# Kernel optimization log

Hardware: AMD Instinct MI355X
Metric: run time of the kernel (lower is better)

The kernel has to match this reference:

```python
import jax, jax.numpy as jnp
import numpy as np
from jax import lax

H = 145; W = 145; BANDS = 200; D_MODEL = 128; NUM_CLASSES = 17
# Mamba2 defaults: expand=2, headdim=64, d_state=128, d_conv=4, ngroups=1
D_INNER = 256; NHEADS = 4; HEADDIM = 64; D_STATE = 128; D_CONV = 4
D_IN_PROJ = 2 * D_INNER + 2 * D_STATE + NHEADS  # 772
CONV_DIM = D_INNER + 2 * D_STATE                # 512


def _gelu(x):
    return jax.nn.gelu(x, approximate=False)


def _ln(x, g, b, eps=1e-5):
    m = jnp.mean(x, -1, keepdims=True)
    v = jnp.mean((x - m) ** 2, -1, keepdims=True)
    return (x - m) * lax.rsqrt(v + eps) * g + b


def _adaptive_pool_last(x, out):
    # PyTorch AdaptiveAvgPool semantics along the last axis via integral image
    L = x.shape[-1]
    i = np.arange(out)
    starts = (i * L) // out
    ends = -((-(i + 1) * L) // out)  # ceil((i+1)*L/out)
    cs = jnp.concatenate([jnp.zeros(x.shape[:-1] + (1,), x.dtype), jnp.cumsum(x, -1)], -1)
    return (cs[..., ends] - cs[..., starts]) / jnp.asarray(ends - starts, x.dtype)


def _mamba2(u, in_w, conv_w, conv_b, dt_bias, A_log, D, norm_w, out_w):
    # u: (L, D_MODEL). Faithful Mamba2 reference path (batch=1 squeezed).
    L = u.shape[0]
    zxbcdt = u @ in_w                      # (L, 772)
    z = zxbcdt[:, :D_INNER]                # (L, 256)
    xBC = zxbcdt[:, D_INNER:2 * D_INNER + 2 * D_STATE]  # (L, 512)
    dt = jax.nn.softplus(zxbcdt[:, -NHEADS:] + dt_bias)  # (L, 4)
    # causal depthwise conv1d, kernel D_CONV, then SiLU
    xp = jnp.pad(xBC, ((D_CONV - 1, 0), (0, 0)))
    xBC = sum(xp[k:k + L] * conv_w[:, k] for k in range(D_CONV)) + conv_b
    xBC = jax.nn.silu(xBC)
    xh = xBC[:, :D_INNER].reshape(L, NHEADS, HEADDIM)     # (L, h, p)
    Bm = xBC[:, D_INNER:D_INNER + D_STATE]                # (L, n)
    Cm = xBC[:, D_INNER + D_STATE:]                       # (L, n)
    A = -jnp.exp(A_log)                                   # (h,)

    def step(state, inp):
        dt_t, x_t, B_t, C_t = inp          # (h,), (h,p), (n,), (n,)
        dA = jnp.exp(dt_t * A)             # (h,)
        state = state * dA[:, None, None] + (dt_t[:, None] * x_t)[:, :, None] * B_t[None, None, :]
        y_t = jnp.einsum('hpn,n->hp', state, C_t)
        return state, y_t

    s0 = jnp.zeros((NHEADS, HEADDIM, D_STATE), u.dtype)
    _, y = lax.scan(step, s0, (dt, xh, Bm, Cm))           # y: (L, h, p)
    y = y + D[None, :, None] * xh
    y = y.reshape(L, D_INNER) * jax.nn.silu(z)            # gated
    y = y * lax.rsqrt(jnp.mean(y * y, -1, keepdims=True) + 1e-5) * norm_w  # RMSNormGated
    return y @ out_w                                      # (L, D_MODEL)


def _forward(x, ln_pre_g, ln_pre_b, fe_w1, fe_b1, fe_w2, fe_b2,
             cv_w1, cv_b1, cv_w2, cv_b2, mp_w, mp_b, mp_ln_g, mp_ln_b,
             m_in_w, m_conv_w, m_conv_b, m_dt_bias, m_A_log, m_D, m_norm_w, m_out_w,
             cls_ln_g, cls_ln_b, cls_w1, cls_b1, cls_w2, cls_b2, cls_w3, cls_b3):
    h, w, _ = x.shape
    xn = _ln(x, ln_pre_g, ln_pre_b)
    # MLP feature branch
    f = _gelu(xn @ fe_w1 + fe_b1)
    f = _gelu(f @ fe_w2 + fe_b2)                          # (h, w, 128)
    # conv branch
    c = jnp.transpose(xn, (2, 0, 1))[None]                # (1, bands, h, w)
    dn = ('NCHW', 'OIHW', 'NCHW')
    c = lax.conv_general_dilated(c, cv_w1, (1, 1), [(2, 2), (2, 2)], dimension_numbers=dn)
    c = _gelu(c + cv_b1[None, :, None, None])             # (1, 32, 147, 147)
    c = lax.conv_general_dilated(c, cv_w2, (1, 1), [(1, 1), (1, 1)], dimension_numbers=dn)
    c = _gelu(c + cv_b2[None, :, None, None])             # (1, 64, 147, 147)
    c = _adaptive_pool_last(c, W)                         # pool width -> 145
    c = _adaptive_pool_last(c.swapaxes(-1, -2), H).swapaxes(-1, -2)  # pool height
    conv_feat = jnp.transpose(c[0], (1, 2, 0))            # (145, 145, 64)
    comb = jnp.concatenate([f, conv_feat], -1).reshape(h * w, 192)
    p = _gelu(_ln(comb @ mp_w + mp_b, mp_ln_g, mp_ln_b))  # (L, d_model)
    m = _mamba2(p, m_in_w, m_conv_w, m_conv_b, m_dt_bias, m_A_log, m_D, m_norm_w, m_out_w)
    r = m.reshape(h, w, D_MODEL)
    o = _ln(r, cls_ln_g, cls_ln_b)
    o = _gelu(o @ cls_w1 + cls_b1)
    o = _gelu(o @ cls_w2 + cls_b2)
    return o @ cls_w3 + cls_b3                            # (h, w, num_classes)


def setup_inputs() -> dict:
    key = jax.random.key(0)
    ks = jax.random.split(key, 16)
    def n(k, shape, s=0.02):
        return jax.random.normal(k, shape, jnp.float32) * s
    return dict(
        x=jax.random.normal(ks[0], (H, W, BANDS), jnp.float32),
        ln_pre_g=jnp.ones((BANDS,), jnp.float32), ln_pre_b=jnp.zeros((BANDS,), jnp.float32),
        fe_w1=n(ks[1], (BANDS, 256)), fe_b1=jnp.zeros((256,), jnp.float32),
        fe_w2=n(ks[2], (256, 128)), fe_b2=jnp.zeros((128,), jnp.float32),
        cv_w1=n(ks[3], (32, BANDS, 3, 3)), cv_b1=jnp.zeros((32,), jnp.float32),
        cv_w2=n(ks[4], (64, 32, 3, 3)), cv_b2=jnp.zeros((64,), jnp.float32),
        mp_w=n(ks[5], (192, D_MODEL)), mp_b=jnp.zeros((D_MODEL,), jnp.float32),
        mp_ln_g=jnp.ones((D_MODEL,), jnp.float32), mp_ln_b=jnp.zeros((D_MODEL,), jnp.float32),
        m_in_w=n(ks[6], (D_MODEL, D_IN_PROJ)),
        m_conv_w=n(ks[7], (CONV_DIM, D_CONV), 0.2), m_conv_b=jnp.zeros((CONV_DIM,), jnp.float32),
        m_dt_bias=jnp.full((NHEADS,), -4.0, jnp.float32),
        m_A_log=jnp.log(jnp.linspace(1.0, 16.0, NHEADS)).astype(jnp.float32),
        m_D=jnp.ones((NHEADS,), jnp.float32),
        m_norm_w=jnp.ones((D_INNER,), jnp.float32),
        m_out_w=n(ks[8], (D_INNER, D_MODEL)),
        cls_ln_g=jnp.ones((D_MODEL,), jnp.float32), cls_ln_b=jnp.zeros((D_MODEL,), jnp.float32),
        cls_w1=n(ks[9], (D_MODEL, 128)), cls_b1=jnp.zeros((128,), jnp.float32),
        cls_w2=n(ks[10], (128, 64)), cls_b2=jnp.zeros((64,), jnp.float32),
        cls_w3=n(ks[11], (64, NUM_CLASSES)), cls_b3=jnp.zeros((NUM_CLASSES,), jnp.float32),
    )


def reference(x, ln_pre_g, ln_pre_b, fe_w1, fe_b1, fe_w2, fe_b2,
              cv_w1, cv_b1, cv_w2, cv_b2, mp_w, mp_b, mp_ln_g, mp_ln_b,
              m_in_w, m_conv_w, m_conv_b, m_dt_bias, m_A_log, m_D, m_norm_w, m_out_w,
              cls_ln_g, cls_ln_b, cls_w1, cls_b1, cls_w2, cls_b2, cls_w3, cls_b3):
    return _forward(x, ln_pre_g, ln_pre_b, fe_w1, fe_b1, fe_w2, fe_b2,
                    cv_w1, cv_b1, cv_w2, cv_b2, mp_w, mp_b, mp_ln_g, mp_ln_b,
                    m_in_w, m_conv_w, m_conv_b, m_dt_bias, m_A_log, m_D, m_norm_w, m_out_w,
                    cls_ln_g, cls_ln_b, cls_w1, cls_b1, cls_w2, cls_b2, cls_w3, cls_b3)
```

## Files before the change

kernel.cpp:

```cpp
#include <hip/hip_runtime.h>
#include <math.h>

#define HW 21025
#define Hdim 145
#define Wdim 145
#define NBANDS 200
#define CONVH 147
#define CONVHW 21609
#define QC 64
#define NCH 329
#define DTP 21056
#define SP 72
#define SSD_GRID 1344
#define NYB165 165

typedef __attribute__((ext_vector_type(4))) float fv4;
typedef __attribute__((ext_vector_type(8))) short short8;

#define OFF_XN   ((size_t)0)
#define OFF_F1   ((size_t)4205000)
#define OFF_COMB ((size_t)9587400)
#define OFF_P    ((size_t)13624200)
#define OFF_ZX   ((size_t)16315400)
#define OFF_XBC  ((size_t)32546700)
#define OFF_S    ((size_t)43311500)
#define OFF_DT   ((size_t)54092172)
#define OFF_CT   ((size_t)54176396)
#define OFF_W    ((size_t)54177712)

__device__ __forceinline__ float gelu_f(float x){
    return 0.5f * x * (1.0f + erff(x * 0.70710678118654752440f));
}
__device__ __forceinline__ float silu_f(float x){
    return x / (1.0f + expf(-x));
}

__device__ __forceinline__ void bf16_split(float x, unsigned short& hs, unsigned short& ls){
    unsigned u = __float_as_uint(x);
    hs = (unsigned short)(u >> 16);
    float hif = __uint_as_float(u & 0xFFFF0000u);
    float lof = x - hif;
    ls = (unsigned short)(__float_as_uint(lof) >> 16);
}
__device__ __forceinline__ unsigned pack2(unsigned short a, unsigned short b){
    return (unsigned)a | ((unsigned)b << 16);
}
__device__ __forceinline__ unsigned packsplit(float x){
    unsigned short hs, ls;
    bf16_split(x, hs, ls);
    return ((unsigned)hs << 16) | (unsigned)ls;
}
__device__ __forceinline__ float unpackf(unsigned u){
    return __uint_as_float(u & 0xFFFF0000u) + __uint_as_float(u << 16);
}
__device__ __forceinline__ void split8g(const float* p, short8& h8, short8& l8){
    fv4 v0 = *reinterpret_cast<const fv4*>(p);
    fv4 v1 = *reinterpret_cast<const fv4*>(p + 4);
    unsigned short hs, ls;
    #pragma unroll
    for (int j = 0; j < 4; j++){
        bf16_split(v0[j], hs, ls); h8[j] = (short)hs; l8[j] = (short)ls;
        bf16_split(v1[j], hs, ls); h8[4 + j] = (short)hs; l8[4 + j] = (short)ls;
    }
}
__device__ __forceinline__ void unpack8(const unsigned* p, short8& h8, short8& l8){
    uint4 a = *reinterpret_cast<const uint4*>(p);
    uint4 b = *reinterpret_cast<const uint4*>(p + 4);
    unsigned v0 = a.x, v1 = a.y, v2 = a.z, v3 = a.w;
    unsigned v4 = b.x, v5 = b.y, v6 = b.z, v7 = b.w;
    h8[0]=(short)(v0>>16); l8[0]=(short)(v0&0xFFFFu);
    h8[1]=(short)(v1>>16); l8[1]=(short)(v1&0xFFFFu);
    h8[2]=(short)(v2>>16); l8[2]=(short)(v2&0xFFFFu);
    h8[3]=(short)(v3>>16); l8[3]=(short)(v3&0xFFFFu);
    h8[4]=(short)(v4>>16); l8[4]=(short)(v4&0xFFFFu);
    h8[5]=(short)(v5>>16); l8[5]=(short)(v5&0xFFFFu);
    h8[6]=(short)(v6>>16); l8[6]=(short)(v6&0xFFFFu);
    h8[7]=(short)(v7>>16); l8[7]=(short)(v7&0xFFFFu);
}

__device__ __forceinline__ bool gemm_decode(int bid, int NXB, int NYB, int& bx, int& by){
    int m = bid & 7;
    int r = bid >> 3;
    bx = r % NXB;
    by = (r / NXB) * 8 + m;
    return by < NYB;
}
__host__ __forceinline__ int gemm_grid(int NXB, int NYB){ return 8 * ((NYB + 7) / 8) * NXB; }

template<int ACT>
__global__ void ln_kernel(const float* __restrict__ in, const float* __restrict__ g,
                          const float* __restrict__ b, float* __restrict__ out, int D){
    int row = blockIdx.x, tid = threadIdx.x;
    const float* r = in + (size_t)row * D;
    float s = 0.f, s2 = 0.f;
    for (int i = tid; i < D; i += 256){ float v = r[i]; s += v; s2 += v*v; }
    __shared__ float r1[4], r2[4];
    #pragma unroll
    for (int o = 32; o > 0; o >>= 1){ s += __shfl_down(s, o); s2 += __shfl_down(s2, o); }
    if ((tid & 63) == 0){ r1[tid >> 6] = s; r2[tid >> 6] = s2; }
    __syncthreads();
    float S = r1[0] + r1[1] + r1[2] + r1[3];
    float S2 = r2[0] + r2[1] + r2[2] + r2[3];
    float mean = S / (float)D;
    float var = S2 / (float)D - mean * mean;
    float rs = rsqrtf(fmaxf(var, 0.f) + 1e-5f);
    float* o_ = out + (size_t)row * D;
    for (int i = tid; i < D; i += 256){
        float v = (r[i] - mean) * rs * g[i] + b[i];
        if (ACT == 1) v = gelu_f(v);
        o_[i] = v;
    }
}

template<int ACT>
__global__ __launch_bounds__(256) void gemm_mfma(const float* __restrict__ A, int lda,
                                                 const float* __restrict__ B,
                                                 const float* __restrict__ bias,
                                                 float* __restrict__ C, int ldc,
                                                 int M, int N, int K, int NXB, int NYB){
    const int SA = 40;
    __shared__ __align__(16) unsigned short Ah[128 * SA], Al[128 * SA];
    __shared__ __align__(16) unsigned short Bh[64 * SA],  Bl[64 * SA];
    int bx, by;
    if (!gemm_decode(blockIdx.x, NXB, NYB, bx, by)) return;
    int tid = threadIdx.x;
    int lane = tid & 63, wid = tid >> 6;
    int wy = wid >> 1, wx = wid & 1;
    int bm = by * 128, bn = bx * 64;
    int l15 = lane & 15, g = lane >> 4;

    fv4 acc[4][2];
    #pragma unroll
    for (int i = 0; i < 4; i++)
        #pragma unroll
        for (int j = 0; j < 2; j++) acc[i][j] = (fv4){0.f,0.f,0.f,0.f};

    int am = tid >> 1;
    int aq = (tid & 1) * 4;
    bool arow_ok = (bm + am) < M;
    int bn_t = tid & 63;
    int bk8 = (tid >> 6) * 8;
    bool bcol_ok = (bn + bn_t) < N;

    int nK = (K + 31) / 32;
    for (int ks = 0; ks < nK; ks++){
        int k0 = ks * 32;
        const float* Ap = A + (size_t)(bm + am) * lda + k0;
        #pragma unroll
        for (int f = 0; f < 4; f++){
            int kq = aq + f;
            fv4 v = (fv4){0.f,0.f,0.f,0.f};
            if (arow_ok && (k0 + kq * 4 + 4) <= K)
                v = *reinterpret_cast<const fv4*>(Ap + kq * 4);
            unsigned short hs[4], ls[4];
            #pragma unroll
            for (int j = 0; j < 4; j++) bf16_split(v[j], hs[j], ls[j]);
            unsigned off = am * SA + kq * 4;
            *reinterpret_cast<uint2*>(&Ah[off]) = make_uint2(pack2(hs[0],hs[1]), pack2(hs[2],hs[3]));
            *reinterpret_cast<uint2*>(&Al[off]) = make_uint2(pack2(ls[0],ls[1]), pack2(ls[2],ls[3]));
        }
        {
            unsigned short hs[8], ls[8];
            #pragma unroll
            for (int j = 0; j < 8; j++){
                int kk = k0 + bk8 + j;
                float v = (bcol_ok && kk < K) ? B[(size_t)kk * N + bn + bn_t] : 0.f;
                bf16_split(v, hs[j], ls[j]);
            }
            unsigned off = bn_t * SA + bk8;
            *reinterpret_cast<uint4*>(&Bh[off]) = make_uint4(pack2(hs[0],hs[1]), pack2(hs[2],hs[3]),
                                                             pack2(hs[4],hs[5]), pack2(hs[6],hs[7]));
            *reinterpret_cast<uint4*>(&Bl[off]) = make_uint4(pack2(ls[0],ls[1]), pack2(ls[2],ls[3]),
                                                             pack2(ls[4],ls[5]), pack2(ls[6],ls[7]));
        }
        __syncthreads();
        short8 afh[4], afl[4], bfh[2], bfl[2];
        #pragma unroll
        for (int mi = 0; mi < 4; mi++){
            unsigned off = (wy * 64 + mi * 16 + l15) * SA + g * 8;
            afh[mi] = *reinterpret_cast<const short8*>(&Ah[off]);
            afl[mi] = *reinterpret_cast<const short8*>(&Al[off]);
        }
        #pragma unroll
        for (int ni = 0; ni < 2; ni++){
            unsigned off = (wx * 32 + ni * 16 + l15) * SA + g * 8;
            bfh[ni] = *reinterpret_cast<const short8*>(&Bh[off]);
            bfl[ni] = *reinterpret_cast<const short8*>(&Bl[off]);
        }
        #pragma unroll
        for (int mi = 0; mi < 4; mi++)
            #pragma unroll
            for (int ni = 0; ni < 2; ni++){
                acc[mi][ni] = __builtin_amdgcn_mfma_f32_16x16x32_bf16(afh[mi], bfh[ni], acc[mi][ni], 0, 0, 0);
                acc[mi][ni] = __builtin_amdgcn_mfma_f32_16x16x32_bf16(afh[mi], bfl[ni], acc[mi][ni], 0, 0, 0);
                acc[mi][ni] = __builtin_amdgcn_mfma_f32_16x16x32_bf16(afl[mi], bfh[ni], acc[mi][ni], 0, 0, 0);
            }
        __syncthreads();
    }
    #pragma unroll
    for (int mi = 0; mi < 4; mi++){
        #pragma unroll
        for (int ni = 0; ni < 2; ni++){
            int cc = bn + wx * 32 + ni * 16 + l15;
            if (cc >= N) continue;
            float bv = bias ? bias[cc] : 0.f;
            #pragma unroll
            for (int j = 0; j < 4; j++){
                int rr = bm + wy * 64 + mi * 16 + g * 4 + j;
                if (rr >= M) continue;
                float v = acc[mi][ni][j] + bv;
                if (ACT == 1) v = gelu_f(v);
                C[(size_t)rr * ldc + cc] = v;
            }
        }
    }
}

template<int IC, int OC, int NCHUNK>
__global__ void prep_w(const float* __restrict__ w, unsigned short* __restrict__ Wh,
                       unsigned short* __restrict__ Wl){
    const int KP = NCHUNK * 288;
    int idx = blockIdx.x * 256 + threadIdx.x;
    if (idx >= OC * KP) return;
    int o = idx / KP, k = idx % KP;
    int ch = k / 288, rest = k % 288, t = rest / 32, c = rest & 31;
    int ci = ch * 32 + c;
    float v = (ci < IC) ? w[((size_t)o * IC + ci) * 9 + t] : 0.f;
    unsigned short hs, ls;
    bf16_split(v, hs, ls);
    Wh[idx] = hs; Wl[idx] = ls;
}

template<int IC, int OC, int PAD, int NCHUNK, int NFRAG>
__global__ __launch_bounds__(256) void conv_mfma(const float* __restrict__ in,
                                                 int inH, int inW,
                                                 const unsigned short* __restrict__ Wh,
                                                 const unsigned short* __restrict__ Wl,
                                                 const float* __restrict__ bias,
                                                 float* __restrict__ out){
    const int KP = NCHUNK * 288;
    const int CST = 40;
    __shared__ __align__(16) unsigned short Xh[3 * 68 * CST], Xl[3 * 68 * CST];
    int y = blockIdx.y;
    int x0 = blockIdx.x * 64;
    int tid = threadIdx.x;
    int lane = tid & 63, wid = tid >> 6;
    int wy = wid >> 1, wx = wid & 1;
    int l15 = lane & 15, g = lane >> 4;

    fv4 acc[2][NFRAG];
    #pragma unroll
    for (int mi = 0; mi < 2; mi++)
        #pragma unroll
        for (int ni = 0; ni < NFRAG; ni++) acc[mi][ni] = (fv4){0.f,0.f,0.f,0.f};

    for (int ch = 0; ch < NCHUNK; ch++){
        int ci0 = ch * 32;
        if (ch > 0) __syncthreads();
        for (int e = tid; e < 3 * 68 * 8; e += 256){
            int qd = e & 7;
            int c  = (e >> 3) % 68;
            int r  = e / 544;
            int iy = y - PAD + r, ix = x0 - PAD + c;
            fv4 v = (fv4){0.f,0.f,0.f,0.f};
            if ((unsigned)iy < (unsigned)inH && (unsigned)ix < (unsigned)inW &&
                (ci0 + qd * 4 + 4) <= IC)
                v = *reinterpret_cast<const fv4*>(in + ((size_t)iy * inW + ix) * IC + ci0 + qd * 4);
            unsigned short hs[4], ls[4];
            #pragma unroll
            for (int j = 0; j < 4; j++) bf16_split(v[j], hs[j], ls[j]);
            unsigned off = (r * 68 + c) * CST + qd * 4;
            *reinterpret_cast<uint2*>(&Xh[off]) = make_uint2(pack2(hs[0],hs[1]), pack2(hs[2],hs[3]));
            *reinterpret_cast<uint2*>(&Xl[off]) = make_uint2(pack2(ls[0],ls[1]), pack2(ls[2],ls[3]));
        }
        __syncthreads();
        #pragma unroll
        for (int t = 0; t < 9; t++){
            int ky = t / 3, kx = t % 3;
            short8 ah[2], al[2], bh[NFRAG], bl[NFRAG];
            #pragma unroll
            for (int mi = 0; mi < 2; mi++){
                unsigned off = (ky * 68 + wy * 32 + mi * 16 + l15 + kx) * CST + g * 8;
                ah[mi] = *reinterpret_cast<const short8*>(&Xh[off]);
                al[mi] = *reinterpret_cast<const short8*>(&Xl[off]);
            }
            #pragma unroll
            for (int ni = 0; ni < NFRAG; ni++){
                int oc = wx * (16 * NFRAG) + ni * 16 + l15;
                size_t woff = (size_t)oc * KP + ch * 288 + t * 32 + g * 8;
                bh[ni] = *reinterpret_cast<const short8*>(&Wh[woff]);
                bl[ni] = *reinterpret_cast<const short8*>(&Wl[woff]);
            }
            #pragma unroll
            for (int mi = 0; mi < 2; mi++)
                #pragma unroll
                for (int ni = 0; ni < NFRAG; ni++){
                    acc[mi][ni] = __builtin_amdgcn_mfma_f32_16x16x32_bf16(ah[mi], bh[ni], acc[mi][ni], 0, 0, 0);
                    acc[mi][ni] = __builtin_amdgcn_mfma_f32_16x16x32_bf16(ah[mi], bl[ni], acc[mi][ni], 0, 0, 0);
                    acc[mi][ni] = __builtin_amdgcn_mfma_f32_16x16x32_bf16(al[mi], bh[ni], acc[mi][ni], 0, 0, 0);
                }
        }
    }
    #pragma unroll
    for (int mi = 0; mi < 2; mi++)
        #pragma unroll
        for (int ni = 0; ni < NFRAG; ni++){
            int oc = wx * (16 * NFRAG) + ni * 16 + l15;
            float bv = bias[oc];
            #pragma unroll
            for (int j = 0; j < 4; j++){
                int x = x0 + wy * 32 + mi * 16 + g * 4 + j;
                if (x >= CONVH) continue;
                out[((size_t)y * CONVH + x) * OC + oc] = gelu_f(acc[mi][ni][j] + bv);
            }
        }
}

__global__ void pool_kernel(const float* __restrict__ c2, float* __restrict__ comb){
    int idx = blockIdx.x * 256 + threadIdx.x;
    if (idx >= HW * 64) return;
    int o = idx & 63;
    int pix = idx >> 6;
    int xo = pix % Wdim, yo = pix / Wdim;
    int ys = yo * CONVH / Hdim, ye = ((yo + 1) * CONVH + Hdim - 1) / Hdim;
    int xs = xo * CONVH / Wdim, xe = ((xo + 1) * CONVH + Wdim - 1) / Wdim;
    float s = 0.f;
    for (int yy = ys; yy < ye; yy++)
        for (int xx = xs; xx < xe; xx++)
            s += c2[((size_t)yy * CONVH + xx) * 64 + o];
    comb[(size_t)pix * 192 + 128 + o] = s / (float)((ye - ys) * (xe - xs));
}

__global__ void dt_kernel(const float* __restrict__ zx, const float* __restrict__ dt_bias,
                          float* __restrict__ dtbT){
    int t = blockIdx.x * 256 + threadIdx.x;
    int h = blockIdx.y;
    if (t >= HW) return;
    float v = zx[(size_t)t * 772 + 768 + h] + dt_bias[h];
    dtbT[h * DTP + t] = (v > 20.f) ? v : log1pf(expf(v));
}

__global__ __launch_bounds__(256) void conv1d_tiled(const float* __restrict__ zx,
                                                    const float* __restrict__ w,
                                                    const float* __restrict__ b,
                                                    unsigned* __restrict__ xbcp){
    __shared__ float xs[67 * 128];
    __shared__ float wc[4 * 128];
    __shared__ float bc[128];
    int t0 = blockIdx.y * 64;
    int c0 = blockIdx.x * 128;
    int tid = threadIdx.x;
    for (int e = tid; e < 67 * 128; e += 256){
        int rr = e >> 7, cc = e & 127;
        int t = t0 - 3 + rr;
        xs[e] = (t >= 0 && t < HW) ? zx[(size_t)t * 772 + 256 + c0 + cc] : 0.f;
    }
    if (tid < 128){
        bc[tid] = b[c0 + tid];
        #pragma unroll
        for (int k = 0; k < 4; k++) wc[k * 128 + tid] = w[(c0 + tid) * 4 + k];
    }
    __syncthreads();
    for (int e = tid; e < 64 * 128; e += 256){
        int tt = e >> 7, cc = e & 127;
        if (t0 + tt >= HW) continue;
        float acc = bc[cc];
        #pragma unroll
        for (int k = 0; k < 4; k++) acc += xs[(tt + k) * 128 + cc] * wc[k * 128 + cc];
        xbcp[(size_t)(t0 + tt) * 512 + c0 + cc] = packsplit(silu_f(acc));
    }
}

__device__ __forceinline__ void chunk_cumsum_t(const float* __restrict__ dtbT, int t0, int Q,
                                               int h, const float* __restrict__ A_log,
                                               float* cum, float* dth){
    int tid = threadIdx.x;
    if (tid < 64){
        float d = (tid < Q) ? dtbT[h * DTP + t0 + tid] : 0.f;
        dth[tid] = d;
        float A = -expf(A_log[h]);
        float a = d * A;
        #pragma unroll
        for (int off = 1; off < 64; off <<= 1){
            float u = __shfl_up(a, off);
            if (tid >= off) a += u;
        }
        cum[tid] = a;
    }
    __syncthreads();
}

__device__ __forceinline__ bool ssd_decode(int bid, int& c, int& h){
    int m = bid & 7, rest = bid >> 3;
    h = rest & 3;
    c = (rest >> 2) * 8 + m;
    return c < NCH;
}

__global__ __launch_bounds__(256) void ssd_phaseA(const unsigned* __restrict__ xbcp,
                                                  const float* __restrict__ dtbT,
                                                  const float* __restrict__ A_log,
                                                  unsigned* __restrict__ Sp,
                                                  float* __restrict__ chunkT){
    __shared__ __align__(16) unsigned short BTh[128 * SP], BTl[128 * SP];
    __shared__ __align__(16) unsigned short XTh[64 * SP],  XTl[64 * SP];
    __shared__ float cum[64], dth[64], wln[64];
    int c, h;
    if (!ssd_decode(blockIdx.x, c, h)) return;
    int t0 = c * QC, Q = min(QC, HW - t0);
    int tid = threadIdx.x;
    chunk_cumsum_t(dtbT, t0, Q, h, A_log, cum, dth);
    float T = cum[Q - 1];
    if (tid == 0) chunkT[c * 4 + h] = T;
    if (tid < 64) wln[tid] = (tid < Q) ? __expf(T - cum[tid]) * dth[tid] : 0.f;
    __syncthreads();
    for (int e2 = tid; e2 < 4096; e2 += 256){
        int nn = e2 & 127, sp = e2 >> 7;
        int s0 = 2 * sp;
        unsigned v0 = (s0 < Q)     ? xbcp[(size_t)(t0 + s0) * 512 + 256 + nn] : 0u;
        unsigned v1 = (s0 + 1 < Q) ? xbcp[(size_t)(t0 + s0 + 1) * 512 + 256 + nn] : 0u;
        *reinterpret_cast<unsigned*>(&BTh[nn * SP + s0]) = pack2((unsigned short)(v0 >> 16), (unsigned short)(v1 >> 16));
        *reinterpret_cast<unsigned*>(&BTl[nn * SP + s0]) = pack2((unsigned short)(v0 & 0xFFFFu), (unsigned short)(v1 & 0xFFFFu));
    }
    for (int e2 = tid; e2 < 2048; e2 += 256){
        int pp = e2 & 63, sp = e2 >> 6;
        int s0 = 2 * sp;
        float v0 = (s0 < Q)     ? unpackf(xbcp[(size_t)(t0 + s0) * 512 + h * 64 + pp]) * wln[s0] : 0.f;
        float v1 = (s0 + 1 < Q) ? unpackf(xbcp[(size_t)(t0 + s0 + 1) * 512 + h * 64 + pp]) * wln[s0 + 1] : 0.f;
        unsigned short h0, l0, h1, l1;
        bf16_split(v0, h0, l0); bf16_split(v1, h1, l1);
        *reinterpret_cast<unsigned*>(&XTh[pp * SP + s0]) = pack2(h0, h1);
        *reinterpret_cast<unsigned*>(&XTl[pp * SP + s0]) = pack2(l0, l1);
    }
    __syncthreads();
    int lane = tid & 63, wid = tid >> 6;
    int wy = wid >> 1, wx = wid & 1;
    int l15 = lane & 15, g = lane >> 4;
    fv4 acc[2][4];
    #pragma unroll
    for (int mi = 0; mi < 2; mi++)
        #pragma unroll
        for (int ni = 0; ni < 4; ni++) acc[mi][ni] = (fv4){0.f,0.f,0.f,0.f};
    #pragma unroll
    for (int ks = 0; ks < 2; ks++){
        short8 ah[2], al[2], bh_[4], bl_[4];
        #pragma unroll
        for (int mi = 0; mi < 2; mi++){
            unsigned off = (wy * 32 + mi * 16 + l15) * SP + ks * 32 + g * 8;
            ah[mi] = *reinterpret_cast<const short8*>(&XTh[off]);
            al[mi] = *reinterpret_cast<const short8*>(&XTl[off]);
        }
        #pragma unroll
        for (int ni = 0; ni < 4; ni++){
            unsigned off = (wx * 64 + ni * 16 + l15) * SP + ks * 32 + g * 8;
            bh_[ni] = *reinterpret_cast<const short8*>(&BTh[off]);
            bl_[ni] = *reinterpret_cast<const short8*>(&BTl[off]);
        }
        #pragma unroll
        for (int mi = 0; mi < 2; mi++)
            #pragma unroll
            for (int ni = 0; ni < 4; ni++){
                acc[mi][ni] = __builtin_amdgcn_mfma_f32_16x16x32_bf16(ah[mi], bh_[ni], acc[mi][ni], 0, 0, 0);
                acc[mi][ni] = __builtin_amdgcn_mfma_f32_16x16x32_bf16(ah[mi], bl_[ni], acc[mi][ni], 0, 0, 0);
                acc[mi][ni] = __builtin_amdgcn_mfma_f32_16x16x32_bf16(al[mi], bh_[ni], acc[mi][ni], 0, 0, 0);
            }
    }
    size_t sb = (size_t)(c * 4 + h) * 8192;
    #pragma unroll
    for (int mi = 0; mi < 2; mi++)
        #pragma unroll
        for (int ni = 0; ni < 4; ni++)
            #pragma unroll
            for (int j = 0; j < 4; j++){
                int p = wy * 32 + mi * 16 + g * 4 + j;
                int n = wx * 64 + ni * 16 + l15;
                Sp[sb + p * 128 + n] = packsplit(acc[mi][ni][j]);
            }
}

__global__ __launch_bounds__(256) void ssd_phaseB(unsigned* __restrict__ Sp,
                                                  const float* __restrict__ chunkT){
    __shared__ float e[NCH];
    int tid = threadIdx.x;
    int idx = blockIdx.x * 256 + tid;
    int h = idx >> 13, pn = idx & 8191;
    for (int c = tid; c < NCH; c += 256) e[c] = __expf(chunkT[c * 4 + h]);
    __syncthreads();
    #define ADDR_(cc) Sp[((size_t)((cc) * 4 + h)) * 8192 + pn]
    unsigned r0 = ADDR_(0), r1 = ADDR_(1), r2 = ADDR_(2), r3 = ADDR_(3);
    float s = 0.f;
    int c = 0;
    for (; c + 8 <= NCH; c += 4){
        unsigned n0 = ADDR_(c + 4), n1 = ADDR_(c + 5), n2 = ADDR_(c + 6), n3 = ADDR_(c + 7);
        ADDR_(c) = packsplit(s);     s = fmaf(s, e[c],     unpackf(r0));
        ADDR_(c + 1) = packsplit(s); s = fmaf(s, e[c + 1], unpackf(r1));
        ADDR_(c + 2) = packsplit(s); s = fmaf(s, e[c + 2], unpackf(r2));
        ADDR_(c + 3) = packsplit(s); s = fmaf(s, e[c + 3], unpackf(r3));
        r0 = n0; r1 = n1; r2 = n2; r3 = n3;
    }
    for (; c < NCH; c++){
        unsigned nx = (c + 4 < NCH) ? ADDR_(c + 4) : 0u;
        float loc = unpackf(r0); r0 = r1; r1 = r2; r2 = r3; r3 = nx;
        ADDR_(c) = packsplit(s);
        s = fmaf(s, e[c], loc);
    }
    #undef ADDR_
}

__global__ __launch_bounds__(256) void ssd_phaseC(const unsigned* __restrict__ xbcp,
                                                  const float* __restrict__ dtbT,
                                                  const float* __restrict__ A_log,
                                                  const float* __restrict__ Dvec,
                                                  const unsigned* __restrict__ Sp,
                                                  float* __restrict__ y){
    __shared__ __align__(16) unsigned short U0h[64 * SP], U0l[64 * SP];
    __shared__ __align__(16) unsigned short U1h[64 * SP], U1l[64 * SP];
    __shared__ float cum[64], dth[64];
    int c, h;
    if (!ssd_decode(blockIdx.x, c, h)) return;
    int t0 = c * QC, Q = min(QC, HW - t0);
    int tid = threadIdx.x;
    chunk_cumsum_t(dtbT, t0, Q, h, A_log, cum, dth);
    int lane = tid & 63, wid = tid >> 6;
    int wy = wid >> 1, wx = wid & 1;
    int l15 = lane & 15, g = lane >> 4;

    int trow[2], srow[2], prow[2];
    #pragma unroll
    for (int i = 0; i < 2; i++){
        trow[i] = min(t0 + wy * 32 + i * 16 + l15, HW - 1);
        srow[i] = min(t0 + wx * 32 + i * 16 + l15, HW - 1);
        prow[i] = wx * 32 + i * 16 + l15;
    }

    fv4 accG[2][2], accA[2][2];
    #pragma unroll
    for (int mi = 0; mi < 2; mi++)
        #pragma unroll
        for (int ni = 0; ni < 2; ni++){ accG[mi][ni] = (fv4){0.f,0.f,0.f,0.f}; accA[mi][ni] = (fv4){0.f,0.f,0.f,0.f}; }

    const unsigned* Sbase = Sp + (size_t)(c * 4 + h) * 8192;
    #pragma unroll
    for (int k0 = 0; k0 < 128; k0 += 32){
        short8 ah[2], al[2], bh[2], bl[2], sh[2], sl[2];
        #pragma unroll
        for (int mi = 0; mi < 2; mi++)
            unpack8(xbcp + (size_t)trow[mi] * 512 + 384 + k0 + g * 8, ah[mi], al[mi]);
        #pragma unroll
        for (int ni = 0; ni < 2; ni++){
            unpack8(xbcp + (size_t)srow[ni] * 512 + 256 + k0 + g * 8, bh[ni], bl[ni]);
            unpack8(Sbase + prow[ni] * 128 + k0 + g * 8, sh[ni], sl[ni]);
        }
        #pragma unroll
        for (int mi = 0; mi < 2; mi++)
            #pragma unroll
            for (int ni = 0; ni < 2; ni++){
                accG[mi][ni] = __builtin_amdgcn_mfma_f32_16x16x32_bf16(ah[mi], bh[ni], accG[mi][ni], 0, 0, 0);
                accG[mi][ni] = __builtin_amdgcn_mfma_f32_16x16x32_bf16(ah[mi], bl[ni], accG[mi][ni], 0, 0, 0);
                accG[mi][ni] = __builtin_amdgcn_mfma_f32_16x16x32_bf16(al[mi], bh[ni], accG[mi][ni], 0, 0, 0);
                accA[mi][ni] = __builtin_amdgcn_mfma_f32_16x16x32_bf16(ah[mi], sh[ni], accA[mi][ni], 0, 0, 0);
                accA[mi][ni] = __builtin_amdgcn_mfma_f32_16x16x32_bf16(ah[mi], sl[ni], accA[mi][ni], 0, 0, 0);
                accA[mi][ni] = __builtin_amdgcn_mfma_f32_16x16x32_bf16(al[mi], sh[ni], accA[mi][ni], 0, 0, 0);
            }
    }
    #pragma unroll
    for (int mi = 0; mi < 2; mi++)
        #pragma unroll
        for (int ni = 0; ni < 2; ni++)
            #pragma unroll
            for (int j = 0; j < 4; j++){
                int t = wy * 32 + mi * 16 + g * 4 + j;
                int s = wx * 32 + ni * 16 + l15;
                float pv = 0.f;
                if (s <= t && s < Q)
                    pv = accG[mi][ni][j] * __expf(cum[t] - cum[s]) * dth[s];
                unsigned short hs, ls;
                bf16_split(pv, hs, ls);
                U0h[t * SP + s] = hs;
                U0l[t * SP + s] = ls;
            }
    for (int e2 = tid; e2 < 2048; e2 += 256){
        int pp = e2 & 63, sp = e2 >> 6;
        int s0 = 2 * sp;
        unsigned v0 = (s0 < Q)     ? xbcp[(size_t)(t0 + s0) * 512 + h * 64 + pp] : 0u;
        unsigned v1 = (s0 + 1 < Q) ? xbcp[(size_t)(t0 + s0 + 1) * 512 + h * 64 + pp] : 0u;
        *reinterpret_cast<unsigned*>(&U1h[pp * SP + s0]) = pack2((unsigned short)(v0 >> 16), (unsigned short)(v1 >> 16));
        *reinterpret_cast<unsigned*>(&U1l[pp * SP + s0]) = pack2((unsigned short)(v0 & 0xFFFFu), (unsigned short)(v1 & 0xFFFFu));
    }
    __syncthreads();
    fv4 accY[2][2];
    #pragma unroll
    for (int mi = 0; mi < 2; mi++)
        #pragma unroll
        for (int ni = 0; ni < 2; ni++)
            #pragma unroll
            for (int j = 0; j < 4; j++){
                int t = wy * 32 + mi * 16 + g * 4 + j;
                accY[mi][ni][j] = __expf(cum[t]) * accA[mi][ni][j];
            }
    #pragma unroll
    for (int kk = 0; kk < 2; kk++){
        short8 ph[2], pl[2], xh[2], xl[2];
        #pragma unroll
        for (int mi = 0; mi < 2; mi++){
            unsigned off = (wy * 32 + mi * 16 + l15) * SP + kk * 32 + g * 8;
            ph[mi] = *reinterpret_cast<const short8*>(&U0h[off]);
            pl[mi] = *reinterpret_cast<const short8*>(&U0l[off]);
        }
        #pragma unroll
        for (int ni = 0; ni < 2; ni++){
            unsigned off = (wx * 32 + ni * 16 + l15) * SP + kk * 32 + g * 8;
            xh[ni] = *reinterpret_cast<const short8*>(&U1h[off]);
            xl[ni] = *reinterpret_cast<const short8*>(&U1l[off]);
        }
        #pragma unroll
        for (int mi = 0; mi < 2; mi++)
            #pragma unroll
            for (int ni = 0; ni < 2; ni++){
                accY[mi][ni] = __builtin_amdgcn_mfma_f32_16x16x32_bf16(ph[mi], xh[ni], accY[mi][ni], 0, 0, 0);
                accY[mi][ni] = __builtin_amdgcn_mfma_f32_16x16x32_bf16(ph[mi], xl[ni], accY[mi][ni], 0, 0, 0);
                accY[mi][ni] = __builtin_amdgcn_mfma_f32_16x16x32_bf16(pl[mi], xh[ni], accY[mi][ni], 0, 0, 0);
            }
    }
    float Dh = Dvec[h];
    #pragma unroll
    for (int mi = 0; mi < 2; mi++)
        #pragma unroll
        for (int ni = 0; ni < 2; ni++)
            #pragma unroll
            for (int j = 0; j < 4; j++){
                int t = wy * 32 + mi * 16 + g * 4 + j;
                if (t >= Q) continue;
                int p = wx * 32 + ni * 16 + l15;
                float xv = unpackf(xbcp[(size_t)(t0 + t) * 512 + h * 64 + p]);
                y[(size_t)(t0 + t) * 256 + h * 64 + p] = accY[mi][ni][j] + Dh * xv;
            }
}

__global__ void gated_rms_kernel(float* __restrict__ y, const float* __restrict__ zx,
                                 const float* __restrict__ nw){
    int row = blockIdx.x, tid = threadIdx.x;
    float v = y[(size_t)row * 256 + tid];
    float z = zx[(size_t)row * 772 + tid];
    v *= silu_f(z);
    float s = v * v;
    __shared__ float r1[4];
    #pragma unroll
    for (int o = 32; o > 0; o >>= 1) s += __shfl_down(s, o);
    if ((tid & 63) == 0) r1[tid >> 6] = s;
    __syncthreads();
    float S = r1[0] + r1[1] + r1[2] + r1[3];
    float rs = rsqrtf(S / 256.f + 1e-5f);
    y[(size_t)row * 256 + tid] = v * rs * nw[tid];
}

extern "C" void kernel_launch(void* const* d_in, const int* in_sizes, int n_in,
                              void* d_out, int out_size, void* d_ws, size_t ws_size,
                              hipStream_t stream){
    (void)in_sizes; (void)n_in; (void)out_size; (void)ws_size;
    const float* x        = (const float*)d_in[0];
    const float* ln_pre_g = (const float*)d_in[1];
    const float* ln_pre_b = (const float*)d_in[2];
    const float* fe_w1    = (const float*)d_in[3];
    const float* fe_b1    = (const float*)d_in[4];
    const float* fe_w2    = (const float*)d_in[5];
    const float* fe_b2    = (const float*)d_in[6];
    const float* cv_w1    = (const float*)d_in[7];
    const float* cv_b1    = (const float*)d_in[8];
    const float* cv_w2    = (const float*)d_in[9];
    const float* cv_b2    = (const float*)d_in[10];
    const float* mp_w     = (const float*)d_in[11];
    const float* mp_b     = (const float*)d_in[12];
    const float* mp_ln_g  = (const float*)d_in[13];
    const float* mp_ln_b  = (const float*)d_in[14];
    const float* m_in_w   = (const float*)d_in[15];
    const float* m_conv_w = (const float*)d_in[16];
    const float* m_conv_b = (const float*)d_in[17];
    const float* m_dtb    = (const float*)d_in[18];
    const float* m_A_log  = (const float*)d_in[19];
    const float* m_D      = (const float*)d_in[20];
    const float* m_norm_w = (const float*)d_in[21];
    const float* m_out_w  = (const float*)d_in[22];
    const float* cls_ln_g = (const float*)d_in[23];
    const float* cls_ln_b = (const float*)d_in[24];
    const float* cls_w1   = (const float*)d_in[25];
    const float* cls_b1   = (const float*)d_in[26];
    const float* cls_w2   = (const float*)d_in[27];
    const float* cls_b2   = (const float*)d_in[28];
    const float* cls_w3   = (const float*)d_in[29];
    const float* cls_b3   = (const float*)d_in[30];

    float* ws   = (float*)d_ws;
    float* xn   = ws + OFF_XN;
    float* f1   = ws + OFF_F1;
    float* comb = ws + OFF_COMB;
    float* p    = ws + OFF_P;
    float* zx   = ws + OFF_ZX;
    unsigned* xbcp = (unsigned*)(ws + OFF_XBC);
    unsigned* Sp = (unsigned*)(ws + OFF_S);
    float* dtbT = ws + OFF_DT;
    float* chkT = ws + OFF_CT;
    float* c1h  = ws + OFF_XBC;
    float* c2h  = ws + OFF_XBC + 691488;
    float* pr   = ws + OFF_XN;
    float* ybuf = ws + OFF_F1;
    float* mo   = ws + OFF_COMB;
    float* cls0 = ws + OFF_XN;
    float* cls1 = ws + OFF_P;
    float* cls2 = ws + OFF_COMB + 2691200;
    unsigned short* W1h = (unsigned short*)(ws + OFF_W);
    unsigned short* W1l = (unsigned short*)(ws + OFF_W + 32256);
    unsigned short* W2h = (unsigned short*)(ws + OFF_W + 64512);
    unsigned short* W2l = (unsigned short*)(ws + OFF_W + 73728);

    prep_w<200, 32, 7><<<(32 * 2016 + 255) / 256, 256, 0, stream>>>(cv_w1, W1h, W1l);
    prep_w<32, 64, 1><<<(64 * 288 + 255) / 256, 256, 0, stream>>>(cv_w2, W2h, W2l);
    ln_kernel<0><<<HW, 256, 0, stream>>>(x, ln_pre_g, ln_pre_b, xn, NBANDS);
    gemm_mfma<1><<<gemm_grid(4, NYB165), 256, 0, stream>>>(xn, 200, fe_w1, fe_b1, f1, 256, HW, 256, 200, 4, NYB165);
    gemm_mfma<1><<<gemm_grid(2, NYB165), 256, 0, stream>>>(f1, 256, fe_w2, fe_b2, comb, 192, HW, 128, 256, 2, NYB165);
    conv_mfma<200, 32, 2, 7, 1><<<dim3(3, CONVH), 256, 0, stream>>>(xn, Hdim, Wdim, W1h, W1l, cv_b1, c1h);
    conv_mfma<32, 64, 1, 1, 2><<<dim3(3, CONVH), 256, 0, stream>>>(c1h, CONVH, CONVH, W2h, W2l, cv_b2, c2h);
    pool_kernel<<<(HW * 64 + 255) / 256, 256, 0, stream>>>(c2h, comb);
    gemm_mfma<0><<<gemm_grid(2, NYB165), 256, 0, stream>>>(comb, 192, mp_w, mp_b, pr, 128, HW, 128, 192, 2, NYB165);
    ln_kernel<1><<<HW, 256, 0, stream>>>(pr, mp_ln_g, mp_ln_b, p, 128);
    gemm_mfma<0><<<gemm_grid(13, NYB165), 256, 0, stream>>>(p, 128, m_in_w, (const float*)nullptr, zx, 772, HW, 772, 128, 13, NYB165);
    dt_kernel<<<dim3((HW + 255) / 256, 4), 256, 0, stream>>>(zx, m_dtb, dtbT);
    conv1d_tiled<<<dim3(4, NCH), 256, 0, stream>>>(zx, m_conv_w, m_conv_b, xbcp);
    ssd_phaseA<<<SSD_GRID, 256, 0, stream>>>(xbcp, dtbT, m_A_log, Sp, chkT);
    ssd_phaseB<<<128, 256, 0, stream>>>(Sp, chkT);
    ssd_phaseC<<<SSD_GRID, 256, 0, stream>>>(xbcp, dtbT, m_A_log, m_D, Sp, ybuf);
    gated_rms_kernel<<<HW, 256, 0, stream>>>(ybuf, zx, m_norm_w);
    gemm_mfma<0><<<gemm_grid(2, NYB165), 256, 0, stream>>>(ybuf, 256, m_out_w, (const float*)nullptr, mo, 128, HW, 128, 256, 2, NYB165);
    ln_kernel<0><<<HW, 256, 0, stream>>>(mo, cls_ln_g, cls_ln_b, cls0, 128);
    gemm_mfma<1><<<gemm_grid(2, NYB165), 256, 0, stream>>>(cls0, 128, cls_w1, cls_b1, cls1, 128, HW, 128, 128, 2, NYB165);
    gemm_mfma<1><<<gemm_grid(1, NYB165), 256, 0, stream>>>(cls1, 128, cls_w2, cls_b2, cls2, 64, HW, 64, 128, 1, NYB165);
    gemm_mfma<0><<<gemm_grid(1, NYB165), 256, 0, stream>>>(cls2, 64, cls_w3, cls_b3, (float*)d_out, 17, HW, 17, 64, 1, NYB165);
}
```

Baseline: 504.1 us.

## Add wide-N MFMA GEMM with fused LayerNorm epilogue and separate dt projection

Adds a GEMM variant with 128-column tiles and a configurable M tile. When a block spans the full 128-wide row, it computes LayerNorm (optionally followed by GELU) in the epilogue. This removes two standalone LayerNorm kernels and their intermediate buffer round-trips. The in_proj GEMM now covers only 768 columns, and the 4 dt columns are computed by a small dot-product kernel straight from p, replacing the old dt_kernel's strided reads of zx. In exchange, tile shapes change for several GEMMs, which shifts occupancy and the amount of redundant B-operand staging.

```diff
diff --git a/kernel.cpp b/kernel.cpp
--- a/kernel.cpp
+++ b/kernel.cpp
@@ -12,7 +12,6 @@
 #define DTP 21056
 #define SP 72
 #define SSD_GRID 1344
-#define NYB165 165
 
 typedef __attribute__((ext_vector_type(4))) float fv4;
 typedef __attribute__((ext_vector_type(8))) short short8;
@@ -109,6 +108,163 @@
         float v = (r[i] - mean) * rs * g[i] + b[i];
         if (ACT == 1) v = gelu_f(v);
         o_[i] = v;
+    }
+}
+
+template<int ACT, int MI>
+__global__ __launch_bounds__(256) void gemm_mfma_w(const float* __restrict__ A, int lda,
+                                                   const float* __restrict__ B, int ldb,
+                                                   const float* __restrict__ bias,
+                                                   const float* __restrict__ lng,
+                                                   const float* __restrict__ lnb,
+                                                   float* __restrict__ C, int ldc,
+                                                   int M, int N, int K, int NXB, int NYB){
+    const int SA = 40;
+    const int BM = MI * 32;
+    __shared__ __align__(16) unsigned short Ah[BM * SA], Al[BM * SA];
+    __shared__ __align__(16) unsigned short Bh[128 * SA], Bl[128 * SA];
+    __shared__ float rs1[2][BM], rs2_[2][BM];
+    int bx, by;
+    if (!gemm_decode(blockIdx.x, NXB, NYB, bx, by)) return;
+    int tid = threadIdx.x;
+    int lane = tid & 63, wid = tid >> 6;
+    int wy = wid >> 1, wx = wid & 1;
+    int bm = by * BM, bn = bx * 128;
+    int l15 = lane & 15, g = lane >> 4;
+
+    fv4 acc[MI][4];
+    #pragma unroll
+    for (int i = 0; i < MI; i++)
+        #pragma unroll
+        for (int j = 0; j < 4; j++) acc[i][j] = (fv4){0.f,0.f,0.f,0.f};
+
+    int bcol = tid & 127;
+    int bk16 = (tid >> 7) * 16;
+    bool bcol_ok = (bn + bcol) < N;
+
+    int nK = (K + 31) / 32;
+    for (int ks = 0; ks < nK; ks++){
+        int k0 = ks * 32;
+        #pragma unroll
+        for (int f = 0; f < MI; f++){
+            int idx = tid * MI + f;
+            int row = idx >> 3, qd = idx & 7;
+            fv4 v = (fv4){0.f,0.f,0.f,0.f};
+            if ((bm + row) < M && (k0 + qd * 4 + 4) <= K)
+                v = *reinterpret_cast<const fv4*>(A + (size_t)(bm + row) * lda + k0 + qd * 4);
+            unsigned short hs[4], ls[4];
+            #pragma unroll
+            for (int j = 0; j < 4; j++) bf16_split(v[j], hs[j], ls[j]);
+            unsigned off = row * SA + qd * 4;
+            *reinterpret_cast<uint2*>(&Ah[off]) = make_uint2(pack2(hs[0],hs[1]), pack2(hs[2],hs[3]));
+            *reinterpret_cast<uint2*>(&Al[off]) = make_uint2(pack2(ls[0],ls[1]), pack2(ls[2],ls[3]));
+        }
+        {
+            unsigned short hs[16], ls[16];
+            #pragma unroll
+            for (int j = 0; j < 16; j++){
+                int kk = k0 + bk16 + j;
+                float v = (bcol_ok && kk < K) ? B[(size_t)kk * ldb + bn + bcol] : 0.f;
+                bf16_split(v, hs[j], ls[j]);
+            }
+            unsigned off = bcol * SA + bk16;
+            *reinterpret_cast<uint4*>(&Bh[off]) = make_uint4(pack2(hs[0],hs[1]), pack2(hs[2],hs[3]),
+                                                             pack2(hs[4],hs[5]), pack2(hs[6],hs[7]));
+            *reinterpret_cast<uint4*>(&Bh[off + 8]) = make_uint4(pack2(hs[8],hs[9]), pack2(hs[10],hs[11]),
+                                                                 pack2(hs[12],hs[13]), pack2(hs[14],hs[15]));
+            *reinterpret_cast<uint4*>(&Bl[off]) = make_uint4(pack2(ls[0],ls[1]), pack2(ls[2],ls[3]),
+                                                             pack2(ls[4],ls[5]), pack2(ls[6],ls[7]));
+            *reinterpret_cast<uint4*>(&Bl[off + 8]) = make_uint4(pack2(ls[8],ls[9]), pack2(ls[10],ls[11]),
+                                                                 pack2(ls[12],ls[13]), pack2(ls[14],ls[15]));
+        }
+        __syncthreads();
+        short8 afh[MI], afl[MI], bfh[4], bfl[4];
+        #pragma unroll
+        for (int mi = 0; mi < MI; mi++){
+            unsigned off = (wy * (MI * 16) + mi * 16 + l15) * SA + g * 8;
+            afh[mi] = *reinterpret_cast<const short8*>(&Ah[off]);
+            afl[mi] = *reinterpret_cast<const short8*>(&Al[off]);
+        }
+        #pragma unroll
+        for (int ni = 0; ni < 4; ni++){
+            unsigned off = (wx * 64 + ni * 16 + l15) * SA + g * 8;
+            bfh[ni] = *reinterpret_cast<const short8*>(&Bh[off]);
+            bfl[ni] = *reinterpret_cast<const short8*>(&Bl[off]);
+        }
+        #pragma unroll
+        for (int mi = 0; mi < MI; mi++)
+            #pragma unroll
+            for (int ni = 0; ni < 4; ni++){
+                acc[mi][ni] = __builtin_amdgcn_mfma_f32_16x16x32_bf16(afh[mi], bfh[ni], acc[mi][ni], 0, 0, 0);
+                acc[mi][ni] = __builtin_amdgcn_mfma_f32_16x16x32_bf16(afh[mi], bfl[ni], acc[mi][ni], 0, 0, 0);
+                acc[mi][ni] = __builtin_amdgcn_mfma_f32_16x16x32_bf16(afl[mi], bfh[ni], acc[mi][ni], 0, 0, 0);
+            }
+        __syncthreads();
+    }
+    float bv[4], lgv[4], lbv[4];
+    #pragma unroll
+    for (int ni = 0; ni < 4; ni++){
+        int cc = bn + wx * 64 + ni * 16 + l15;
+        bool ok = cc < N;
+        bv[ni]  = (bias && ok) ? bias[cc] : 0.f;
+        if (ACT >= 2){ lgv[ni] = ok ? lng[cc] : 1.f; lbv[ni] = ok ? lnb[cc] : 0.f; }
+    }
+    if (ACT >= 2){
+        #pragma unroll
+        for (int mi = 0; mi < MI; mi++)
+            #pragma unroll
+            for (int j = 0; j < 4; j++){
+                float s = 0.f, s2 = 0.f;
+                #pragma unroll
+                for (int ni = 0; ni < 4; ni++){
+                    float v = acc[mi][ni][j] + bv[ni];
+                    s += v; s2 += v * v;
+                }
+                #pragma unroll
+                for (int o = 1; o < 16; o <<= 1){
+                    s += __shfl_xor(s, o); s2 += __shfl_xor(s2, o);
+                }
+                int row = wy * (MI * 16) + mi * 16 + g * 4 + j;
+                if (l15 == 0){ rs1[wx][row] = s; rs2_[wx][row] = s2; }
+            }
+        __syncthreads();
+        #pragma unroll
+        for (int mi = 0; mi < MI; mi++)
+            #pragma unroll
+            for (int j = 0; j < 4; j++){
+                int row = wy * (MI * 16) + mi * 16 + g * 4 + j;
+                int rr = bm + row;
+                if (rr >= M) continue;
+                float S = rs1[0][row] + rs1[1][row];
+                float S2 = rs2_[0][row] + rs2_[1][row];
+                float mean = S / 128.f;
+                float var = S2 / 128.f - mean * mean;
+                float rsq = rsqrtf(fmaxf(var, 0.f) + 1e-5f);
+                #pragma unroll
+                for (int ni = 0; ni < 4; ni++){
+                    int cc = bn + wx * 64 + ni * 16 + l15;
+                    float v = acc[mi][ni][j] + bv[ni];
+                    v = (v - mean) * rsq * lgv[ni] + lbv[ni];
+                    if (ACT == 3) v = gelu_f(v);
+                    C[(size_t)rr * ldc + cc] = v;
+                }
+            }
+    } else {
+        #pragma unroll
+        for (int mi = 0; mi < MI; mi++)
+            #pragma unroll
+            for (int ni = 0; ni < 4; ni++){
+                int cc = bn + wx * 64 + ni * 16 + l15;
+                if (cc >= N) continue;
+                #pragma unroll
+                for (int j = 0; j < 4; j++){
+                    int rr = bm + wy * (MI * 16) + mi * 16 + g * 4 + j;
+                    if (rr >= M) continue;
+                    float v = acc[mi][ni][j] + bv[ni];
+                    if (ACT == 1) v = gelu_f(v);
+                    C[(size_t)rr * ldc + cc] = v;
+                }
+            }
     }
 }
 
@@ -216,6 +372,30 @@
     }
 }
 
+__global__ __launch_bounds__(256) void dt_from_p(const float* __restrict__ p,
+                                                 const float* __restrict__ w,
+                                                 const float* __restrict__ dtb,
+                                                 float* __restrict__ dtbT){
+    __shared__ float wl[512];
+    int tid = threadIdx.x;
+    for (int i = tid; i < 512; i += 256){
+        int k = i >> 2, h = i & 3;
+        wl[i] = w[(size_t)k * 772 + 768 + h];
+    }
+    __syncthreads();
+    int t = blockIdx.x * 64 + (tid >> 2);
+    int h = tid & 3;
+    if (t >= HW) return;
+    const float* pr = p + (size_t)t * 128;
+    float s = 0.f;
+    for (int k = 0; k < 128; k += 4){
+        fv4 v = *reinterpret_cast<const fv4*>(pr + k);
+        s += v[0]*wl[k*4+h] + v[1]*wl[(k+1)*4+h] + v[2]*wl[(k+2)*4+h] + v[3]*wl[(k+3)*4+h];
+    }
+    s += dtb[h];
+    dtbT[h * DTP + t] = (s > 20.f) ? s : log1pf(expf(s));
+}
+
 template<int IC, int OC, int NCHUNK>
 __global__ void prep_w(const float* __restrict__ w, unsigned short* __restrict__ Wh,
                        unsigned short* __restrict__ Wl){
@@ -329,15 +509,6 @@
         for (int xx = xs; xx < xe; xx++)
             s += c2[((size_t)yy * CONVH + xx) * 64 + o];
     comb[(size_t)pix * 192 + 128 + o] = s / (float)((ye - ys) * (xe - xs));
-}
-
-__global__ void dt_kernel(const float* __restrict__ zx, const float* __restrict__ dt_bias,
-                          float* __restrict__ dtbT){
-    int t = blockIdx.x * 256 + threadIdx.x;
-    int h = blockIdx.y;
-    if (t >= HW) return;
-    float v = zx[(size_t)t * 772 + 768 + h] + dt_bias[h];
-    dtbT[h * DTP + t] = (v > 20.f) ? v : log1pf(expf(v));
 }
 
 __global__ __launch_bounds__(256) void conv1d_tiled(const float* __restrict__ zx,
@@ -702,9 +873,7 @@
     float* chkT = ws + OFF_CT;
     float* c1h  = ws + OFF_XBC;
     float* c2h  = ws + OFF_XBC + 691488;
-    float* pr   = ws + OFF_XN;
     float* ybuf = ws + OFF_F1;
-    float* mo   = ws + OFF_COMB;
     float* cls0 = ws + OFF_XN;
     float* cls1 = ws + OFF_P;
     float* cls2 = ws + OFF_COMB + 2691200;
@@ -716,23 +885,28 @@
     prep_w<200, 32, 7><<<(32 * 2016 + 255) / 256, 256, 0, stream>>>(cv_w1, W1h, W1l);
     prep_w<32, 64, 1><<<(64 * 288 + 255) / 256, 256, 0, stream>>>(cv_w2, W2h, W2l);
     ln_kernel<0><<<HW, 256, 0, stream>>>(x, ln_pre_g, ln_pre_b, xn, NBANDS);
-    gemm_mfma<1><<<gemm_grid(4, NYB165), 256, 0, stream>>>(xn, 200, fe_w1, fe_b1, f1, 256, HW, 256, 200, 4, NYB165);
-    gemm_mfma<1><<<gemm_grid(2, NYB165), 256, 0, stream>>>(f1, 256, fe_w2, fe_b2, comb, 192, HW, 128, 256, 2, NYB165);
+    gemm_mfma_w<1, 4><<<gemm_grid(2, 165), 256, 0, stream>>>(xn, 200, fe_w1, 256, fe_b1,
+        (const float*)nullptr, (const float*)nullptr, f1, 256, HW, 256, 200, 2, 165);
+    gemm_mfma_w<1, 2><<<gemm_grid(1, 329), 256, 0, stream>>>(f1, 256, fe_w2, 128, fe_b2,
+        (const float*)nullptr, (const float*)nullptr, comb, 192, HW, 128, 256, 1, 329);
     conv_mfma<200, 32, 2, 7, 1><<<dim3(3, CONVH), 256, 0, stream>>>(xn, Hdim, Wdim, W1h, W1l, cv_b1, c1h);
     conv_mfma<32, 64, 1, 1, 2><<<dim3(3, CONVH), 256, 0, stream>>>(c1h, CONVH, CONVH, W2h, W2l, cv_b2, c2h);
     pool_kernel<<<(HW * 64 + 255) / 256, 256, 0, stream>>>(c2h, comb);
-    gemm_mfma<0><<<gemm_grid(2, NYB165), 256, 0, stream>>>(comb, 192, mp_w, mp_b, pr, 128, HW, 128, 192, 2, NYB165);
-    ln_kernel<1><<<HW, 256, 0, stream>>>(pr, mp_ln_g, mp_ln_b, p, 128);
-    gemm_mfma<0><<<gemm_grid(13, NYB165), 256, 0, stream>>>(p, 128, m_in_w, (const float*)nullptr, zx, 772, HW, 772, 128, 13, NYB165);
-    dt_kernel<<<dim3((HW + 255) / 256, 4), 256, 0, stream>>>(zx, m_dtb, dtbT);
+    gemm_mfma_w<3, 2><<<gemm_grid(1, 329), 256, 0, stream>>>(comb, 192, mp_w, 128, mp_b,
+        mp_ln_g, mp_ln_b, p, 128, HW, 128, 192, 1, 329);
+    gemm_mfma_w<0, 4><<<gemm_grid(6, 165), 256, 0, stream>>>(p, 128, m_in_w, 772,
+        (const float*)nullptr, (const float*)nullptr, (const float*)nullptr,
+        zx, 772, HW, 768, 128, 6, 165);
+    dt_from_p<<<(HW + 63) / 64, 256, 0, stream>>>(p, m_in_w, m_dtb, dtbT);
     conv1d_tiled<<<dim3(4, NCH), 256, 0, stream>>>(zx, m_conv_w, m_conv_b, xbcp);
     ssd_phaseA<<<SSD_GRID, 256, 0, stream>>>(xbcp, dtbT, m_A_log, Sp, chkT);
     ssd_phaseB<<<128, 256, 0, stream>>>(Sp, chkT);
     ssd_phaseC<<<SSD_GRID, 256, 0, stream>>>(xbcp, dtbT, m_A_log, m_D, Sp, ybuf);
     gated_rms_kernel<<<HW, 256, 0, stream>>>(ybuf, zx, m_norm_w);
-    gemm_mfma<0><<<gemm_grid(2, NYB165), 256, 0, stream>>>(ybuf, 256, m_out_w, (const float*)nullptr, mo, 128, HW, 128, 256, 2, NYB165);
-    ln_kernel<0><<<HW, 256, 0, stream>>>(mo, cls_ln_g, cls_ln_b, cls0, 128);
-    gemm_mfma<1><<<gemm_grid(2, NYB165), 256, 0, stream>>>(cls0, 128, cls_w1, cls_b1, cls1, 128, HW, 128, 128, 2, NYB165);
-    gemm_mfma<1><<<gemm_grid(1, NYB165), 256, 0, stream>>>(cls1, 128, cls_w2, cls_b2, cls2, 64, HW, 64, 128, 1, NYB165);
-    gemm_mfma<0><<<gemm_grid(1, NYB165), 256, 0, stream>>>(cls2, 64, cls_w3, cls_b3, (float*)d_out, 17, HW, 17, 64, 1, NYB165);
-}
+    gemm_mfma_w<2, 2><<<gemm_grid(1, 329), 256, 0, stream>>>(ybuf, 256, m_out_w, 128,
+        (const float*)nullptr, cls_ln_g, cls_ln_b, cls0, 128, HW, 128, 256, 1, 329);
+    gemm_mfma_w<1, 2><<<gemm_grid(1, 329), 256, 0, stream>>>(cls0, 128, cls_w1, 128, cls_b1,
+        (const float*)nullptr, (const float*)nullptr, cls1, 128, HW, 128, 128, 1, 329);
+    gemm_mfma<1><<<gemm_grid(1, 165), 256, 0, stream>>>(cls1, 128, cls_w2, cls_b2, cls2, 64, HW, 64, 128, 1, 165);
+    gemm_mfma<0><<<gemm_grid(1, 165), 256, 0, stream>>>(cls2, 64, cls_w3, cls_b3, (float*)d_out, 17, HW, 17, 64, 1, 165);
+}
```

Result: faster. 474.9 us (-5.8%).
